# Kernel tuning notes

Measured on AMD Instinct MI355X. Metric: run time of the kernel, lower is better.

## Reference

```python
import jax, jax.numpy as jnp
import numpy as np

B, N, D, U = 8, 4096, 128, 1024


def setup_inputs() -> dict:
    key = jax.random.key(0)
    kx, kw = jax.random.split(key)
    x = jax.random.normal(kx, (B, N, D), dtype=jnp.float32)
    # learned kernel, shape (dims, units) as in build()
    w = jax.random.normal(kw, (D, U), dtype=jnp.float32)
    return {"x": x, "w": w}


def reference(x, w):
    # Squared Euclidean distance from every point x[b,n,:] to every prototype
    # column w[:,u]: sum_d (x[b,n,d] - w[d,u])^2.
    # work is a single GEMM instead of materializing a [B,N,D,U] tensor.
    x2 = jnp.sum(x * x, axis=-1, keepdims=True)        # [B, N, 1]
    w2 = jnp.sum(w * w, axis=0)                        # [U]
    xw = jnp.einsum("bnd,du->bnu", x, w)               # [B, N, U]
    a = x2 + w2 - 2.0 * xw                             # [B, N, U]
    # inverted=False, activation=None -> return raw squared distances
    return a
```

## Files before the change

kernel.cpp:

```cpp
#include <hip/hip_runtime.h>

#define M_TOT 32768
#define K_DIM 128
#define U_TOT 1024

#define GBM 64
#define GBN 128
#define NMS 8

typedef short s16x8 __attribute__((ext_vector_type(8)));
typedef float f32x16 __attribute__((ext_vector_type(16)));

__device__ inline unsigned int f2bf(float f) {
    union { float f; unsigned int u; } v; v.f = f;
    return (v.u + 0x7FFFu + ((v.u >> 16) & 1u)) >> 16;
}

__device__ inline void async_load16(const void* g, void* l) {
    __builtin_amdgcn_global_load_lds((const __attribute__((address_space(1))) void*)g,
                                     (__attribute__((address_space(3))) void*)l,
                                     16, 0, 0);
}

__global__ __launch_bounds__(256) void prep_kernel(
    const float* __restrict__ x, const float* __restrict__ w,
    unsigned int* __restrict__ xb, unsigned int* __restrict__ wt,
    float* __restrict__ x2, float* __restrict__ w2)
{
    const int lane = threadIdx.x & 63;
    const int lc = lane & 31;
    if (blockIdx.x < 4096) {
        const int wv = threadIdx.x >> 6;
        const int row = (blockIdx.x << 3) + (wv << 1) + (lane >> 5);
        const float4 v = ((const float4*)(x + (size_t)row * K_DIM))[lc];
        float s = v.x * v.x + v.y * v.y + v.z * v.z + v.w * v.w;
        #pragma unroll
        for (int off = 16; off; off >>= 1) s += __shfl_xor(s, off);
        uint2 pk;
        pk.x = f2bf(v.x) | (f2bf(v.y) << 16);
        pk.y = f2bf(v.z) | (f2bf(v.w) << 16);
        ((uint2*)xb)[(size_t)row * 32 + lc] = pk;
        if (lc == 0) x2[row] = s;
    } else {
        const int u = ((blockIdx.x - 4096) << 2) + (threadIdx.x >> 6);
        const float a = w[(size_t)(2 * lane) * U_TOT + u];
        const float b = w[(size_t)(2 * lane + 1) * U_TOT + u];
        float s = a * a + b * b;
        #pragma unroll
        for (int off = 32; off; off >>= 1) s += __shfl_xor(s, off);
        wt[u * 64 + lane] = f2bf(a) | (f2bf(b) << 16);
        if (lane == 0) w2[u] = s;
    }
}

__global__ __launch_bounds__(512, 4) void gemm_kernel(
    const unsigned short* __restrict__ xb, const unsigned short* __restrict__ wt,
    const float* __restrict__ x2, const float* __restrict__ w2,
    float* __restrict__ out)
{
    __shared__ __align__(16) unsigned short Bs[GBN * K_DIM];
    __shared__ __align__(16) unsigned short As[2][GBM * K_DIM];

    const int tid = threadIdx.x;
    const int wv = tid >> 6;
    const int lane = tid & 63;
    const int lc = lane & 31;
    const int hi = lane >> 5;

    const int b = blockIdx.x;
    const int ut = (b >> 3) & 7;
    const int msb = (b & 7) * 8 + (b >> 6);
    const int u0 = ut * GBN;
    const int mbase = msb * (GBM * NMS);

    #pragma unroll
    for (int i = 0; i < 4; ++i) {
        const int p = (wv * 4 + i) * 64 + lane;
        const int row = p >> 4;
        const int j = (p & 15) ^ (row & 15);
        async_load16(wt + ((size_t)(u0 + row) << 7) + j * 8, &Bs[(p & ~63) * 8]);
    }
    #pragma unroll
    for (int i = 0; i < 2; ++i) {
        const int p = (wv * 2 + i) * 64 + lane;
        const int row = p >> 4;
        const int j = (p & 15) ^ (row & 15);
        async_load16(xb + ((size_t)(mbase + row) << 7) + j * 8, &As[0][(p & ~63) * 8]);
    }

    const int wr = wv >> 2;
    const int wc = wv & 3;
    const float w2v = w2[u0 + wc * 32 + lc];

    __syncthreads();

    s16x8 bfrag[8];
    #pragma unroll
    for (int st = 0; st < 8; ++st) {
        const int row = wc * 32 + lc;
        const int j0 = (st << 1) + hi;
        bfrag[st] = *(const s16x8*)&Bs[((row << 4) + (j0 ^ (row & 15))) * 8];
    }

    #pragma unroll
    for (int ms = 0; ms < NMS; ++ms) {
        if (ms + 1 < NMS) {
            #pragma unroll
            for (int i = 0; i < 2; ++i) {
                const int p = (wv * 2 + i) * 64 + lane;
                const int row = p >> 4;
                const int j = (p & 15) ^ (row & 15);
                async_load16(xb + ((size_t)(mbase + (ms + 1) * GBM + row) << 7) + j * 8,
                             &As[(ms + 1) & 1][(p & ~63) * 8]);
            }
        }

        const int mb = mbase + ms * GBM + wr * 32;
        const float x2row = x2[mb + lc];

        f32x16 acc = {};
        #pragma unroll
        for (int st = 0; st < 8; ++st) {
            const int row = wr * 32 + lc;
            const int j0 = (st << 1) + hi;
            const s16x8 af = *(const s16x8*)&As[ms & 1][((row << 4) + (j0 ^ (row & 15))) * 8];
            acc = __builtin_amdgcn_mfma_f32_32x32x16_bf16(af, bfrag[st], acc, 0, 0, 0);
        }

        float* op = out + (size_t)mb * U_TOT + u0 + wc * 32 + lc;
        #pragma unroll
        for (int r = 0; r < 16; ++r) {
            const int t = (r & 3) + ((r >> 2) << 3);
            const float xs = __shfl(x2row, t + (hi << 2) + (lane & 32));
            op[(size_t)(t + (hi << 2)) * U_TOT] = xs + w2v - 2.0f * acc[r];
        }
        if (ms + 1 < NMS) __syncthreads();
    }
}

__global__ __launch_bounds__(256) void fallback_kernel(
    const float* __restrict__ x, const float* __restrict__ w,
    float* __restrict__ out)
{
    __shared__ float xrow[K_DIM];
    const int m = blockIdx.x;
    const int tid = threadIdx.x;
    if (tid < K_DIM) xrow[tid] = x[(size_t)m * K_DIM + tid];
    __syncthreads();
    float x2 = 0.f;
    #pragma unroll
    for (int k = 0; k < K_DIM; ++k) x2 += xrow[k] * xrow[k];
    #pragma unroll
    for (int uu = 0; uu < 4; ++uu) {
        const int u = uu * 256 + tid;
        float dot = 0.f, w2 = 0.f;
        for (int k = 0; k < K_DIM; ++k) {
            const float wv = w[(size_t)k * U_TOT + u];
            dot += xrow[k] * wv;
            w2 += wv * wv;
        }
        out[(size_t)m * U_TOT + u] = x2 + w2 - 2.0f * dot;
    }
}

extern "C" void kernel_launch(void* const* d_in, const int* in_sizes, int n_in,
                              void* d_out, int out_size, void* d_ws, size_t ws_size,
                              hipStream_t stream) {
    const float* x = (const float*)d_in[0];
    const float* w = (const float*)d_in[1];
    float* out = (float*)d_out;

    const size_t need = (size_t)M_TOT * K_DIM * 2 + (size_t)U_TOT * K_DIM * 2
                      + (size_t)M_TOT * 4 + (size_t)U_TOT * 4;
    if (ws_size < need) {
        fallback_kernel<<<M_TOT, 256, 0, stream>>>(x, w, out);
        return;
    }

    unsigned short* xb = (unsigned short*)d_ws;
    unsigned short* wt = xb + (size_t)M_TOT * K_DIM;
    float* x2 = (float*)(wt + (size_t)U_TOT * K_DIM);
    float* w2 = x2 + M_TOT;

    prep_kernel<<<4096 + 256, 256, 0, stream>>>(x, w, (unsigned int*)xb,
                                                (unsigned int*)wt, x2, w2);
    gemm_kernel<<<(M_TOT / (GBM * NMS)) * (U_TOT / GBN), 512, 0, stream>>>(xb, wt, x2, w2, out);
}
```

Baseline: 152.4 us.

## Drop LDS staging and load GEMM fragments directly from global memory

Removes the shared-memory buffers, async global-to-LDS loads and block barriers, and has each wave read its A and B MFMA fragments straight from global memory into registers. The tile shrinks to 64 units wide with 256-thread blocks, which doubles the grid. This removes LDS traffic and synchronisation, but gives up cross-wave reuse of the A tile and the prefetch overlap, so reads become uncoalesced strided 16-byte loads that depend on L2.

```diff
diff --git a/kernel.cpp b/kernel.cpp
--- a/kernel.cpp
+++ b/kernel.cpp
@@ -5,7 +5,7 @@
 #define U_TOT 1024
 
 #define GBM 64
-#define GBN 128
+#define GBN 64
 #define NMS 8
 
 typedef short s16x8 __attribute__((ext_vector_type(8)));
@@ -14,12 +14,6 @@
 __device__ inline unsigned int f2bf(float f) {
     union { float f; unsigned int u; } v; v.f = f;
     return (v.u + 0x7FFFu + ((v.u >> 16) & 1u)) >> 16;
-}
-
-__device__ inline void async_load16(const void* g, void* l) {
-    __builtin_amdgcn_global_load_lds((const __attribute__((address_space(1))) void*)g,
-                                     (__attribute__((address_space(3))) void*)l,
-                                     16, 0, 0);
 }
 
 __global__ __launch_bounds__(256) void prep_kernel(
@@ -53,88 +47,57 @@
     }
 }
 
-__global__ __launch_bounds__(512, 4) void gemm_kernel(
+__global__ __launch_bounds__(256, 4) void gemm_kernel(
     const unsigned short* __restrict__ xb, const unsigned short* __restrict__ wt,
     const float* __restrict__ x2, const float* __restrict__ w2,
     float* __restrict__ out)
 {
-    __shared__ __align__(16) unsigned short Bs[GBN * K_DIM];
-    __shared__ __align__(16) unsigned short As[2][GBM * K_DIM];
-
     const int tid = threadIdx.x;
     const int wv = tid >> 6;
     const int lane = tid & 63;
     const int lc = lane & 31;
     const int hi = lane >> 5;
+    const int wr = wv >> 1;
+    const int wc = wv & 1;
 
     const int b = blockIdx.x;
-    const int ut = (b >> 3) & 7;
-    const int msb = (b & 7) * 8 + (b >> 6);
+    const int t = b >> 3;
+    const int ut = t & 15;
+    const int msb = (b & 7) * 8 + (t >> 4);
     const int u0 = ut * GBN;
     const int mbase = msb * (GBM * NMS);
 
-    #pragma unroll
-    for (int i = 0; i < 4; ++i) {
-        const int p = (wv * 4 + i) * 64 + lane;
-        const int row = p >> 4;
-        const int j = (p & 15) ^ (row & 15);
-        async_load16(wt + ((size_t)(u0 + row) << 7) + j * 8, &Bs[(p & ~63) * 8]);
-    }
-    #pragma unroll
-    for (int i = 0; i < 2; ++i) {
-        const int p = (wv * 2 + i) * 64 + lane;
-        const int row = p >> 4;
-        const int j = (p & 15) ^ (row & 15);
-        async_load16(xb + ((size_t)(mbase + row) << 7) + j * 8, &As[0][(p & ~63) * 8]);
-    }
-
-    const int wr = wv >> 2;
-    const int wc = wv & 3;
-    const float w2v = w2[u0 + wc * 32 + lc];
-
-    __syncthreads();
-
+    const unsigned short* wp = wt + ((size_t)(u0 + wc * 32 + lc) << 7) + (hi << 3);
     s16x8 bfrag[8];
     #pragma unroll
-    for (int st = 0; st < 8; ++st) {
-        const int row = wc * 32 + lc;
-        const int j0 = (st << 1) + hi;
-        bfrag[st] = *(const s16x8*)&Bs[((row << 4) + (j0 ^ (row & 15))) * 8];
-    }
+    for (int st = 0; st < 8; ++st)
+        bfrag[st] = *(const s16x8*)(wp + (st << 4));
+
+    const float w2v = w2[u0 + wc * 32 + lc];
 
     #pragma unroll
     for (int ms = 0; ms < NMS; ++ms) {
-        if (ms + 1 < NMS) {
-            #pragma unroll
-            for (int i = 0; i < 2; ++i) {
-                const int p = (wv * 2 + i) * 64 + lane;
-                const int row = p >> 4;
-                const int j = (p & 15) ^ (row & 15);
-                async_load16(xb + ((size_t)(mbase + (ms + 1) * GBM + row) << 7) + j * 8,
-                             &As[(ms + 1) & 1][(p & ~63) * 8]);
-            }
-        }
+        const int mb = mbase + ms * GBM + wr * 32;
+        const unsigned short* ap = xb + ((size_t)(mb + lc) << 7) + (hi << 3);
+        const float x2row = x2[mb + lc];
 
-        const int mb = mbase + ms * GBM + wr * 32;
-        const float x2row = x2[mb + lc];
+        s16x8 af[8];
+        #pragma unroll
+        for (int st = 0; st < 8; ++st)
+            af[st] = *(const s16x8*)(ap + (st << 4));
 
         f32x16 acc = {};
         #pragma unroll
-        for (int st = 0; st < 8; ++st) {
-            const int row = wr * 32 + lc;
-            const int j0 = (st << 1) + hi;
-            const s16x8 af = *(const s16x8*)&As[ms & 1][((row << 4) + (j0 ^ (row & 15))) * 8];
-            acc = __builtin_amdgcn_mfma_f32_32x32x16_bf16(af, bfrag[st], acc, 0, 0, 0);
-        }
+        for (int st = 0; st < 8; ++st)
+            acc = __builtin_amdgcn_mfma_f32_32x32x16_bf16(af[st], bfrag[st], acc, 0, 0, 0);
 
         float* op = out + (size_t)mb * U_TOT + u0 + wc * 32 + lc;
         #pragma unroll
         for (int r = 0; r < 16; ++r) {
-            const int t = (r & 3) + ((r >> 2) << 3);
-            const float xs = __shfl(x2row, t + (hi << 2) + (lane & 32));
-            op[(size_t)(t + (hi << 2)) * U_TOT] = xs + w2v - 2.0f * acc[r];
+            const int tt = (r & 3) + ((r >> 2) << 3);
+            const float xs = __shfl(x2row, tt + (hi << 2) + (lane & 32));
+            op[(size_t)(tt + (hi << 2)) * U_TOT] = xs + w2v - 2.0f * acc[r];
         }
-        if (ms + 1 < NMS) __syncthreads();
     }
 }
 
@@ -184,5 +147,5 @@
 
     prep_kernel<<<4096 + 256, 256, 0, stream>>>(x, w, (unsigned int*)xb,
                                                 (unsigned int*)wt, x2, w2);
-    gemm_kernel<<<(M_TOT / (GBM * NMS)) * (U_TOT / GBN), 512, 0, stream>>>(xb, wt, x2, w2, out);
+    gemm_kernel<<<(M_TOT / (GBM * NMS)) * (U_TOT / GBN), 256, 0, stream>>>(xb, wt, x2, w2, out);
 }
```

Measured after the change: 201.2 us. 32.0% more time.

## Halve GEMM block to 4 waves, each computing two 32x32 MFMA tiles

Applied to the files above, without the earlier changes.

The GEMM block drops from 8 waves to 4. Each wave now covers a 32x64 output tile with two accumulators that share one A fragment per k-step, and the cooperative async loads are remapped so 256 threads fill the same LDS tiles. This halves A-fragment LDS reads per MFMA and gives each wave two independent MFMA chains. In exchange, B-fragment and accumulator register use doubles, there are fewer waves per CU to hide store latency, and launch bounds change from (512,4) to (256,2).

```diff
diff --git a/kernel.cpp b/kernel.cpp
--- a/kernel.cpp
+++ b/kernel.cpp
@@ -53,7 +53,7 @@
     }
 }
 
-__global__ __launch_bounds__(512, 4) void gemm_kernel(
+__global__ __launch_bounds__(256, 2) void gemm_kernel(
     const unsigned short* __restrict__ xb, const unsigned short* __restrict__ wt,
     const float* __restrict__ x2, const float* __restrict__ w2,
     float* __restrict__ out)
@@ -66,6 +66,8 @@
     const int lane = tid & 63;
     const int lc = lane & 31;
     const int hi = lane >> 5;
+    const int wr = wv >> 1;
+    const int wc2 = wv & 1;
 
     const int b = blockIdx.x;
     const int ut = (b >> 3) & 7;
@@ -74,65 +76,71 @@
     const int mbase = msb * (GBM * NMS);
 
     #pragma unroll
-    for (int i = 0; i < 4; ++i) {
-        const int p = (wv * 4 + i) * 64 + lane;
+    for (int i = 0; i < 8; ++i) {
+        const int p = i * 256 + tid;
         const int row = p >> 4;
         const int j = (p & 15) ^ (row & 15);
-        async_load16(wt + ((size_t)(u0 + row) << 7) + j * 8, &Bs[(p & ~63) * 8]);
+        async_load16(wt + ((size_t)(u0 + row) << 7) + j * 8,
+                     &Bs[(i * 256 + (tid & 192)) * 8]);
     }
     #pragma unroll
-    for (int i = 0; i < 2; ++i) {
-        const int p = (wv * 2 + i) * 64 + lane;
+    for (int i = 0; i < 4; ++i) {
+        const int p = i * 256 + tid;
         const int row = p >> 4;
         const int j = (p & 15) ^ (row & 15);
-        async_load16(xb + ((size_t)(mbase + row) << 7) + j * 8, &As[0][(p & ~63) * 8]);
+        async_load16(xb + ((size_t)(mbase + row) << 7) + j * 8,
+                     &As[0][(i * 256 + (tid & 192)) * 8]);
     }
 
-    const int wr = wv >> 2;
-    const int wc = wv & 3;
-    const float w2v = w2[u0 + wc * 32 + lc];
+    const float w2v0 = w2[u0 + wc2 * 64 + lc];
+    const float w2v1 = w2[u0 + wc2 * 64 + 32 + lc];
 
     __syncthreads();
 
-    s16x8 bfrag[8];
+    s16x8 bfr0[8], bfr1[8];
     #pragma unroll
     for (int st = 0; st < 8; ++st) {
-        const int row = wc * 32 + lc;
         const int j0 = (st << 1) + hi;
-        bfrag[st] = *(const s16x8*)&Bs[((row << 4) + (j0 ^ (row & 15))) * 8];
+        const int r0 = wc2 * 64 + lc;
+        const int r1 = wc2 * 64 + 32 + lc;
+        bfr0[st] = *(const s16x8*)&Bs[((r0 << 4) + (j0 ^ (r0 & 15))) * 8];
+        bfr1[st] = *(const s16x8*)&Bs[((r1 << 4) + (j0 ^ (r1 & 15))) * 8];
     }
 
     #pragma unroll
     for (int ms = 0; ms < NMS; ++ms) {
         if (ms + 1 < NMS) {
             #pragma unroll
-            for (int i = 0; i < 2; ++i) {
-                const int p = (wv * 2 + i) * 64 + lane;
+            for (int i = 0; i < 4; ++i) {
+                const int p = i * 256 + tid;
                 const int row = p >> 4;
                 const int j = (p & 15) ^ (row & 15);
                 async_load16(xb + ((size_t)(mbase + (ms + 1) * GBM + row) << 7) + j * 8,
-                             &As[(ms + 1) & 1][(p & ~63) * 8]);
+                             &As[(ms + 1) & 1][(i * 256 + (tid & 192)) * 8]);
             }
         }
 
         const int mb = mbase + ms * GBM + wr * 32;
         const float x2row = x2[mb + lc];
 
-        f32x16 acc = {};
+        f32x16 acc0 = {}, acc1 = {};
         #pragma unroll
         for (int st = 0; st < 8; ++st) {
             const int row = wr * 32 + lc;
             const int j0 = (st << 1) + hi;
             const s16x8 af = *(const s16x8*)&As[ms & 1][((row << 4) + (j0 ^ (row & 15))) * 8];
-            acc = __builtin_amdgcn_mfma_f32_32x32x16_bf16(af, bfrag[st], acc, 0, 0, 0);
+            acc0 = __builtin_amdgcn_mfma_f32_32x32x16_bf16(af, bfr0[st], acc0, 0, 0, 0);
+            acc1 = __builtin_amdgcn_mfma_f32_32x32x16_bf16(af, bfr1[st], acc1, 0, 0, 0);
         }
 
-        float* op = out + (size_t)mb * U_TOT + u0 + wc * 32 + lc;
+        float* op = out + (size_t)mb * U_TOT + u0 + wc2 * 64 + lc;
         #pragma unroll
         for (int r = 0; r < 16; ++r) {
             const int t = (r & 3) + ((r >> 2) << 3);
-            const float xs = __shfl(x2row, t + (hi << 2) + (lane & 32));
-            op[(size_t)(t + (hi << 2)) * U_TOT] = xs + w2v - 2.0f * acc[r];
+            const int tt = t + (hi << 2);
+            const float xs = __shfl(x2row, tt + (lane & 32));
+            op[(size_t)tt * U_TOT]      = xs + w2v0 - 2.0f * acc0[r];
+            op[(size_t)tt * U_TOT + 32] = xs + w2v1 - 2.0f * acc1[r];
         }
         if (ms + 1 < NMS) __syncthreads();
     }
@@ -184,5 +192,5 @@
 
     prep_kernel<<<4096 + 256, 256, 0, stream>>>(x, w, (unsigned int*)xb,
                                                 (unsigned int*)wt, x2, w2);
-    gemm_kernel<<<(M_TOT / (GBM * NMS)) * (U_TOT / GBN), 512, 0, stream>>>(xb, wt, x2, w2, out);
+    gemm_kernel<<<(M_TOT / (GBM * NMS)) * (U_TOT / GBN), 256, 0, stream>>>(xb, wt, x2, w2, out);
 }
```

Result: no change. 152.1 us (-0.2%).
